# Performance work log

Measured on AMD Instinct MI355X. Metric: run time of the kernel, lower is better.

Reference implementation:

```python
import jax, jax.numpy as jnp
import numpy as np

PI = jnp.pi


def _spow(t, p):
    # t >= 0; safe t**p with value 0 (and zero grad) at t == 0
    tt = jnp.where(t > 0, t, 1.0)
    return jnp.where(t > 0, tt ** p, 0.0)


def _wavelets(t, f, fm, pm, em, fo, ph):
    # t: [L]; f: [S,1] -> returns [S, L] bank of wavelets (one per scale)
    sigma = jnp.maximum(fm / (2.0 * PI * f), 1e-6)        # [S,1]
    br = jnp.cos(2.0 * PI * f * t)                        # [S,L]
    bi = jnp.sin(2.0 * PI * f * t)
    # real_part: + pm0*br - c^2 (t/sig)^fo0 br pm1 + ... alternating, c = 2..7
    real = br * pm[0]
    sign = -1.0
    for j in range(6):
        c = j + 2.0
        real = real + sign * (_spow(t, fo[j]) * c / sigma ** fo[j] * c) * br * pm[j + 1]
        sign = -sign
    # imag_part: same pattern with fo6..fo11, pm8..pm13; j==9 term has the
    # anomalous parenthesization from the source: t**fo*5/(sigma**fo*5)
    imag = bi * pm[7]
    sign = -1.0
    for j in range(6, 12):
        c = j - 4.0
        if j == 9:
            term = (_spow(t, fo[j]) * 5.0 / (sigma ** fo[j] * 5.0)) * bi * pm[j + 2]
        else:
            term = (_spow(t, fo[j]) * c / sigma ** fo[j] * c) * bi * pm[j + 2]
        imag = imag + sign * term
        sign = -sign
    gauss = em[0] * jnp.exp(-t ** 2 / (2.0 * sigma ** 2))  # [S,L]
    rw = real * gauss
    iw = imag * gauss
    amp = rw + iw
    samp = amp / jnp.linalg.norm(amp, axis=-1, keepdims=True)
    phase = jnp.arctan2(iw, rw)
    w = (samp * jnp.sin(phase) * ph[0]) * (samp * jnp.cos(phase) * ph[1]) \
        * (samp * jnp.sinc(phase / PI) * ph[2])
    return w


def reference(x, scales, f_mod, poly_mod, exp_mod, frac_order, phase_mod, i):
    B, C = x.shape[0], x.shape[1]
    xf = x.reshape(B, C, -1)                              # [B,C,L]
    L = xf.shape[-1]
    S = scales.shape[0]
    t = jnp.arange(L, dtype=x.dtype)
    f = (1.0 / scales)[:, None]                           # [S,1]
    W = _wavelets(t, f, f_mod[i], poly_mod[i], exp_mod[i], frac_order[i],
                  phase_mod[i])                            # [S,L] kernels, K = L
    # torch F.conv1d(padding='same', groups=C*S) = cross-correlation with
    # left pad (K-1)//2. Computed exactly via zero-padded FFT linear conv.
    K = L
    Nfft = 2 * L                                          # >= L + K - 1, no aliasing
    Xf = jnp.fft.rfft(xf, n=Nfft, axis=-1)                # [B,C,F]
    Wf = jnp.fft.rfft(W[:, ::-1], n=Nfft, axis=-1)        # [S,F] (corr = conv w/ flip)
    y = jnp.fft.irfft(Xf[:, :, None, :] * Wf[None, None], n=Nfft, axis=-1)  # [B,C,S,2L]
    left = (K - 1) // 2
    off = K - 1 - left
    y = y[..., off:off + L]                               # [B,C,S,L]
    # torch channel layout: out[:, j] = corr(x[:, j % C], wavelet[j % S])
    j = jnp.arange(C * S)
    return y[:, j % C, j % S, :]                          # [B, C*S, L]


def setup_inputs() -> dict:
    key = jax.random.key(0)
    ks = jax.random.split(key, 6)
    B, C, H, Wd = 16, 16, 64, 64
    S, NSTEPS = 16, 10
    x = jax.random.normal(ks[0], (B, C, H, Wd), dtype=jnp.float32)
    scales = jnp.linspace(1.0, 32.0, S, dtype=jnp.float32)
    f_mod = 1.0 + 0.02 * jax.random.normal(ks[1], (NSTEPS,), dtype=jnp.float32)
    poly_mod = 1.0 + 0.02 * jax.random.normal(ks[2], (NSTEPS, 14), dtype=jnp.float32)
    exp_mod = 1.0 + 0.02 * jax.random.normal(ks[3], (NSTEPS, 1), dtype=jnp.float32)
    frac_order = 1.0 + 0.02 * jax.random.normal(ks[4], (NSTEPS, 12), dtype=jnp.float32)
    phase_mod = 1.0 + 0.02 * jax.random.normal(ks[5], (NSTEPS, 3), dtype=jnp.float32)
    return {"x": x, "scales": scales, "f_mod": f_mod, "poly_mod": poly_mod,
            "exp_mod": exp_mod, "frac_order": frac_order,
            "phase_mod": phase_mod, "i": 3}
```

## Files before the change

### kernel.cpp

```cpp
#include <hip/hip_runtime.h>
#include <math.h>

#define QMAX 128
#define ZCUT 1920
#define XPAD 127
#define XLEN 2176
#define XS_SZ 2304

typedef float vfloat4 __attribute__((ext_vector_type(4)));

__global__ __launch_bounds__(512) void conv_diag(const float* __restrict__ x,
                                                 const float* __restrict__ scales,
                                                 const float* __restrict__ f_mod,
                                                 const float* __restrict__ poly_mod,
                                                 const float* __restrict__ exp_mod,
                                                 const float* __restrict__ frac_order,
                                                 const float* __restrict__ phase_mod,
                                                 const int* __restrict__ istep,
                                                 float* __restrict__ ws) {
    __shared__ __attribute__((aligned(16))) float xs[XS_SZ];
    __shared__ __attribute__((aligned(16))) float Wl[QMAX];
    __shared__ float wsum[2];

    const int bk = blockIdx.x;
    const int k = bk & 15;
    const int tid = threadIdx.x;

    const float* xrow = x + (size_t)bk * 4096;
    for (int li = tid; li < XS_SZ; li += 512) {
        xs[li] = (li >= XPAD && li < XPAD + XLEN) ? xrow[li - XPAD] : 0.0f;
    }

    float amp = 0.0f, rw = 0.0f, iw = 0.0f;
    if (tid < QMAX) {
        const int i = istep[0];
        const float PI2 = 6.28318530717958647692f;
        const float f = 1.0f / scales[k];
        const float fm = f_mod[i];
        const float* pm = poly_mod + i * 14;
        const float em0 = exp_mod[i];
        const float* fo = frac_order + i * 12;

        const float sigma = fmaxf(fm / (PI2 * f), 1e-6f);
        const float tf = (float)tid;
        const float arg = PI2 * f * tf;
        const float br = cosf(arg);
        const float bi = sinf(arg);

        float rp = pm[0];
        float sign = -1.0f;
        for (int j = 0; j < 6; ++j) {
            float c = (float)(j + 2);
            float sp = (tf > 0.0f) ? powf(tf, fo[j]) : 0.0f;
            rp += sign * (sp * c / powf(sigma, fo[j]) * c * pm[j + 1]);
            sign = -sign;
        }
        float ipoly = pm[7];
        sign = -1.0f;
        for (int j = 6; j < 12; ++j) {
            float sp = (tf > 0.0f) ? powf(tf, fo[j]) : 0.0f;
            float term;
            if (j == 9) {
                term = sp * 5.0f / (powf(sigma, fo[j]) * 5.0f) * pm[j + 2];
            } else {
                float c = (float)(j - 4);
                term = sp * c / powf(sigma, fo[j]) * c * pm[j + 2];
            }
            ipoly += sign * term;
            sign = -sign;
        }

        const float gauss = em0 * expf(-tf * tf / (2.0f * sigma * sigma));
        rw = br * rp * gauss;
        iw = bi * ipoly * gauss;
        amp = rw + iw;

        float sq = amp * amp;
        #pragma unroll
        for (int off = 32; off > 0; off >>= 1) sq += __shfl_xor(sq, off, 64);
        if ((tid & 63) == 0) wsum[tid >> 6] = sq;
    }
    __syncthreads();

    if (tid < QMAX) {
        const int i = istep[0];
        const float* ph = phase_mod + i * 3;
        const float norm = sqrtf(wsum[0] + wsum[1]);
        const float samp = amp / norm;
        const float phase = atan2f(iw, rw);
        const float sphi = sinf(phase);
        const float cphi = cosf(phase);
        const float snc = (phase != 0.0f) ? (sphi / phase) : 1.0f;
        Wl[tid] = (samp * sphi * ph[0]) * (samp * cphi * ph[1]) * (samp * snc * ph[2]);
    }
    __syncthreads();

    float* wrow = ws + (size_t)bk * 4096;
    #pragma unroll
    for (int v = 0; v < 2; ++v) {
        const int fidx = tid + 512 * v;
        const int p = 4 * fidx;
        float4 val = make_float4(0.0f, 0.0f, 0.0f, 0.0f);
        if (p >= ZCUT) {
            float acc[4] = {0.0f, 0.0f, 0.0f, 0.0f};
            const int base = p - 1920;
            float4 xcur = *(const float4*)&xs[base];
            for (int q = 0; q < QMAX; q += 4) {
                float4 w4 = *(const float4*)&Wl[q];
                float4 xnxt = *(const float4*)&xs[base + q + 4];
                float win[8] = {xcur.x, xcur.y, xcur.z, xcur.w,
                                xnxt.x, xnxt.y, xnxt.z, xnxt.w};
                float wv[4] = {w4.x, w4.y, w4.z, w4.w};
                #pragma unroll
                for (int j = 0; j < 4; ++j) {
                    #pragma unroll
                    for (int r = 0; r < 4; ++r) {
                        acc[r] = fmaf(win[r + j], wv[j], acc[r]);
                    }
                }
                xcur = xnxt;
            }
            val = make_float4(acc[0], acc[1], acc[2], acc[3]);
        }
        *(float4*)&wrow[p] = val;
    }
}

__global__ __launch_bounds__(256) void replicate_rows(const float* __restrict__ ws,
                                                      float* __restrict__ out) {
    const int m = blockIdx.x;
    const int b = m >> 8;
    const int j = m & 255;
    const int k = j & 15;
    const float* __restrict__ src = ws + ((size_t)b * 16 + k) * 4096;
    float* __restrict__ dst = out + (size_t)m * 4096;
    const int tid = threadIdx.x;
    #pragma unroll
    for (int v = 0; v < 4; ++v) {
        const int e = 4 * (tid + 256 * v);
        vfloat4 val = (e >= ZCUT) ? *(const vfloat4*)&src[e]
                                  : (vfloat4){0.0f, 0.0f, 0.0f, 0.0f};
        __builtin_nontemporal_store(val, (vfloat4*)&dst[e]);
    }
}

extern "C" void kernel_launch(void* const* d_in, const int* in_sizes, int n_in,
                              void* d_out, int out_size, void* d_ws, size_t ws_size,
                              hipStream_t stream) {
    const float* x          = (const float*)d_in[0];
    const float* scales     = (const float*)d_in[1];
    const float* f_mod      = (const float*)d_in[2];
    const float* poly_mod   = (const float*)d_in[3];
    const float* exp_mod    = (const float*)d_in[4];
    const float* frac_order = (const float*)d_in[5];
    const float* phase_mod  = (const float*)d_in[6];
    const int*   istep      = (const int*)d_in[7];
    float* out = (float*)d_out;
    float* wsd = (float*)d_ws;

    conv_diag<<<dim3(256), dim3(512), 0, stream>>>(
        x, scales, f_mod, poly_mod, exp_mod, frac_order, phase_mod, istep, wsd);

    replicate_rows<<<dim3(4096), dim3(256), 0, stream>>>(wsd, out);
}
```

Before: 35.54 us.

## Split wavelet build into its own kernel, halve conv blocks, batch row replication

Wavelet construction moves out of the convolution kernel into a tiny 16-block kernel, so each conv block no longer recomputes the wavelet with its pow/trig-heavy math. The convolution is split into two half-row blocks of 256 threads, each computing only the nonzero output region and never writing the leading zeros, which doubles block count and shrinks the shared-memory window. Row replication now handles 8 output rows per block instead of one. The cost is an extra kernel launch and a dependency between the three stages.

```diff
diff --git a/kernel.cpp b/kernel.cpp
--- a/kernel.cpp
+++ b/kernel.cpp
@@ -3,144 +3,153 @@
 
 #define QMAX 128
 #define ZCUT 1920
-#define XPAD 127
-#define XLEN 2176
-#define XS_SZ 2304
+#define HALF 1088
+#define XWIN 1216
+#define XS_SZ 1280
 
 typedef float vfloat4 __attribute__((ext_vector_type(4)));
 
-__global__ __launch_bounds__(512) void conv_diag(const float* __restrict__ x,
-                                                 const float* __restrict__ scales,
-                                                 const float* __restrict__ f_mod,
-                                                 const float* __restrict__ poly_mod,
-                                                 const float* __restrict__ exp_mod,
-                                                 const float* __restrict__ frac_order,
-                                                 const float* __restrict__ phase_mod,
-                                                 const int* __restrict__ istep,
+__global__ void wavelet_build(const float* __restrict__ scales,
+                              const float* __restrict__ f_mod,
+                              const float* __restrict__ poly_mod,
+                              const float* __restrict__ exp_mod,
+                              const float* __restrict__ frac_order,
+                              const float* __restrict__ phase_mod,
+                              const int* __restrict__ istep,
+                              float* __restrict__ Wout) {
+    const int k = blockIdx.x;
+    const int t = threadIdx.x;
+    const int i = istep[0];
+    const float PI2 = 6.28318530717958647692f;
+
+    const float f = 1.0f / scales[k];
+    const float fm = f_mod[i];
+    const float* pm = poly_mod + i * 14;
+    const float em0 = exp_mod[i];
+    const float* fo = frac_order + i * 12;
+    const float* ph = phase_mod + i * 3;
+
+    const float sigma = fmaxf(fm / (PI2 * f), 1e-6f);
+    const float tf = (float)t;
+    const float arg = PI2 * f * tf;
+    const float br = cosf(arg);
+    const float bi = sinf(arg);
+
+    float rp = pm[0];
+    float sign = -1.0f;
+    for (int j = 0; j < 6; ++j) {
+        float c = (float)(j + 2);
+        float sp = (tf > 0.0f) ? powf(tf, fo[j]) : 0.0f;
+        rp += sign * (sp * c / powf(sigma, fo[j]) * c * pm[j + 1]);
+        sign = -sign;
+    }
+    float ipoly = pm[7];
+    sign = -1.0f;
+    for (int j = 6; j < 12; ++j) {
+        float sp = (tf > 0.0f) ? powf(tf, fo[j]) : 0.0f;
+        float term;
+        if (j == 9) {
+            term = sp * 5.0f / (powf(sigma, fo[j]) * 5.0f) * pm[j + 2];
+        } else {
+            float c = (float)(j - 4);
+            term = sp * c / powf(sigma, fo[j]) * c * pm[j + 2];
+        }
+        ipoly += sign * term;
+        sign = -sign;
+    }
+
+    const float gauss = em0 * expf(-tf * tf / (2.0f * sigma * sigma));
+    const float rw = br * rp * gauss;
+    const float iw = bi * ipoly * gauss;
+    const float amp = rw + iw;
+
+    float sq = amp * amp;
+    #pragma unroll
+    for (int off = 32; off > 0; off >>= 1) sq += __shfl_xor(sq, off, 64);
+    __shared__ float wsum[2];
+    if ((t & 63) == 0) wsum[t >> 6] = sq;
+    __syncthreads();
+    const float norm = sqrtf(wsum[0] + wsum[1]);
+
+    const float samp = amp / norm;
+    const float phase = atan2f(iw, rw);
+    const float sphi = sinf(phase);
+    const float cphi = cosf(phase);
+    const float snc = (phase != 0.0f) ? (sphi / phase) : 1.0f;
+    Wout[k * QMAX + t] = (samp * sphi * ph[0]) * (samp * cphi * ph[1]) * (samp * snc * ph[2]);
+}
+
+__global__ __launch_bounds__(256) void conv_half(const float* __restrict__ x,
+                                                 const float* __restrict__ W,
                                                  float* __restrict__ ws) {
     __shared__ __attribute__((aligned(16))) float xs[XS_SZ];
     __shared__ __attribute__((aligned(16))) float Wl[QMAX];
-    __shared__ float wsum[2];
 
-    const int bk = blockIdx.x;
+    const int blk = blockIdx.x;
+    const int bk = blk >> 1;
+    const int h = blk & 1;
     const int k = bk & 15;
     const int tid = threadIdx.x;
+    const int Ph = ZCUT + h * HALF;
+
+    if (tid < QMAX) Wl[tid] = W[k * QMAX + tid];
 
     const float* xrow = x + (size_t)bk * 4096;
-    for (int li = tid; li < XS_SZ; li += 512) {
-        xs[li] = (li >= XPAD && li < XPAD + XLEN) ? xrow[li - XPAD] : 0.0f;
-    }
-
-    float amp = 0.0f, rw = 0.0f, iw = 0.0f;
-    if (tid < QMAX) {
-        const int i = istep[0];
-        const float PI2 = 6.28318530717958647692f;
-        const float f = 1.0f / scales[k];
-        const float fm = f_mod[i];
-        const float* pm = poly_mod + i * 14;
-        const float em0 = exp_mod[i];
-        const float* fo = frac_order + i * 12;
-
-        const float sigma = fmaxf(fm / (PI2 * f), 1e-6f);
-        const float tf = (float)tid;
-        const float arg = PI2 * f * tf;
-        const float br = cosf(arg);
-        const float bi = sinf(arg);
-
-        float rp = pm[0];
-        float sign = -1.0f;
-        for (int j = 0; j < 6; ++j) {
-            float c = (float)(j + 2);
-            float sp = (tf > 0.0f) ? powf(tf, fo[j]) : 0.0f;
-            rp += sign * (sp * c / powf(sigma, fo[j]) * c * pm[j + 1]);
-            sign = -sign;
-        }
-        float ipoly = pm[7];
-        sign = -1.0f;
-        for (int j = 6; j < 12; ++j) {
-            float sp = (tf > 0.0f) ? powf(tf, fo[j]) : 0.0f;
-            float term;
-            if (j == 9) {
-                term = sp * 5.0f / (powf(sigma, fo[j]) * 5.0f) * pm[j + 2];
-            } else {
-                float c = (float)(j - 4);
-                term = sp * c / powf(sigma, fo[j]) * c * pm[j + 2];
-            }
-            ipoly += sign * term;
-            sign = -sign;
-        }
-
-        const float gauss = em0 * expf(-tf * tf / (2.0f * sigma * sigma));
-        rw = br * rp * gauss;
-        iw = bi * ipoly * gauss;
-        amp = rw + iw;
-
-        float sq = amp * amp;
-        #pragma unroll
-        for (int off = 32; off > 0; off >>= 1) sq += __shfl_xor(sq, off, 64);
-        if ((tid & 63) == 0) wsum[tid >> 6] = sq;
-    }
-    __syncthreads();
-
-    if (tid < QMAX) {
-        const int i = istep[0];
-        const float* ph = phase_mod + i * 3;
-        const float norm = sqrtf(wsum[0] + wsum[1]);
-        const float samp = amp / norm;
-        const float phase = atan2f(iw, rw);
-        const float sphi = sinf(phase);
-        const float cphi = cosf(phase);
-        const float snc = (phase != 0.0f) ? (sphi / phase) : 1.0f;
-        Wl[tid] = (samp * sphi * ph[0]) * (samp * cphi * ph[1]) * (samp * snc * ph[2]);
+    const int x0 = Ph - 2047;
+    for (int li = tid; li < XS_SZ; li += 256) {
+        int g = x0 + li;
+        xs[li] = (g >= 0 && li < XWIN) ? xrow[g] : 0.0f;
     }
     __syncthreads();
 
     float* wrow = ws + (size_t)bk * 4096;
     #pragma unroll
-    for (int v = 0; v < 2; ++v) {
-        const int fidx = tid + 512 * v;
-        const int p = 4 * fidx;
-        float4 val = make_float4(0.0f, 0.0f, 0.0f, 0.0f);
-        if (p >= ZCUT) {
-            float acc[4] = {0.0f, 0.0f, 0.0f, 0.0f};
-            const int base = p - 1920;
-            float4 xcur = *(const float4*)&xs[base];
-            for (int q = 0; q < QMAX; q += 4) {
-                float4 w4 = *(const float4*)&Wl[q];
-                float4 xnxt = *(const float4*)&xs[base + q + 4];
-                float win[8] = {xcur.x, xcur.y, xcur.z, xcur.w,
-                                xnxt.x, xnxt.y, xnxt.z, xnxt.w};
-                float wv[4] = {w4.x, w4.y, w4.z, w4.w};
+    for (int e = 0; e < 2; ++e) {
+        const int fi = tid + e * 256;
+        if (e == 1 && fi >= HALF / 4) break;
+        const int p = Ph + 4 * fi;
+        const int base = 4 * fi;
+        float acc[4] = {0.0f, 0.0f, 0.0f, 0.0f};
+        float4 xcur = *(const float4*)&xs[base];
+        for (int q = 0; q < QMAX; q += 4) {
+            float4 w4 = *(const float4*)&Wl[q];
+            float4 xnxt = *(const float4*)&xs[base + q + 4];
+            float win[8] = {xcur.x, xcur.y, xcur.z, xcur.w,
+                            xnxt.x, xnxt.y, xnxt.z, xnxt.w};
+            float wv[4] = {w4.x, w4.y, w4.z, w4.w};
+            #pragma unroll
+            for (int j = 0; j < 4; ++j) {
                 #pragma unroll
-                for (int j = 0; j < 4; ++j) {
-                    #pragma unroll
-                    for (int r = 0; r < 4; ++r) {
-                        acc[r] = fmaf(win[r + j], wv[j], acc[r]);
-                    }
+                for (int r = 0; r < 4; ++r) {
+                    acc[r] = fmaf(win[r + j], wv[j], acc[r]);
                 }
-                xcur = xnxt;
             }
-            val = make_float4(acc[0], acc[1], acc[2], acc[3]);
+            xcur = xnxt;
         }
-        *(float4*)&wrow[p] = val;
+        *(float4*)&wrow[p] = make_float4(acc[0], acc[1], acc[2], acc[3]);
     }
 }
 
 __global__ __launch_bounds__(256) void replicate_rows(const float* __restrict__ ws,
                                                       float* __restrict__ out) {
-    const int m = blockIdx.x;
-    const int b = m >> 8;
-    const int j = m & 255;
-    const int k = j & 15;
-    const float* __restrict__ src = ws + ((size_t)b * 16 + k) * 4096;
-    float* __restrict__ dst = out + (size_t)m * 4096;
+    const int g = blockIdx.x;
+    const int m0 = g * 8;
+    const int b = m0 >> 8;
     const int tid = threadIdx.x;
+    const vfloat4 zero = {0.0f, 0.0f, 0.0f, 0.0f};
+
     #pragma unroll
-    for (int v = 0; v < 4; ++v) {
-        const int e = 4 * (tid + 256 * v);
-        vfloat4 val = (e >= ZCUT) ? *(const vfloat4*)&src[e]
-                                  : (vfloat4){0.0f, 0.0f, 0.0f, 0.0f};
-        __builtin_nontemporal_store(val, (vfloat4*)&dst[e]);
+    for (int r = 0; r < 8; ++r) {
+        const int m = m0 + r;
+        const int k = m & 15;
+        const float* __restrict__ src = ws + ((size_t)b * 16 + k) * 4096;
+        float* __restrict__ dst = out + (size_t)m * 4096;
+        #pragma unroll
+        for (int v = 0; v < 4; ++v) {
+            const int e = 4 * (tid + 256 * v);
+            vfloat4 val = (e >= ZCUT) ? *(const vfloat4*)&src[e] : zero;
+            __builtin_nontemporal_store(val, (vfloat4*)&dst[e]);
+        }
     }
 }
 
@@ -157,9 +166,13 @@
     const int*   istep      = (const int*)d_in[7];
     float* out = (float*)d_out;
     float* wsd = (float*)d_ws;
+    float* Wtab = wsd;
+    float* rows = wsd + 4096;
 
-    conv_diag<<<dim3(256), dim3(512), 0, stream>>>(
-        x, scales, f_mod, poly_mod, exp_mod, frac_order, phase_mod, istep, wsd);
+    wavelet_build<<<dim3(16), dim3(QMAX), 0, stream>>>(
+        scales, f_mod, poly_mod, exp_mod, frac_order, phase_mod, istep, Wtab);
 
-    replicate_rows<<<dim3(4096), dim3(256), 0, stream>>>(wsd, out);
+    conv_half<<<dim3(512), dim3(256), 0, stream>>>(x, Wtab, rows);
+
+    replicate_rows<<<dim3(512), dim3(256), 0, stream>>>(rows, out);
 }
```

After: 41.46 us. 1.17x slower.
